# Kernel optimization log

Measured on AMD Instinct MI355X. Metric: run time of the kernel, lower is better.

## Reference

```python
import jax, jax.numpy as jnp
import numpy as np

B, S, E, D = 2, 1024, 1024, 2048
H, KV, HD = 8, 4, 256
SOFTCAP = 50.0
SCALE = 256.0 ** -0.5  # query_pre_attn_scalar ** -0.5
WINDOW = 512
EPS = 1e-6
THETA = 10000.0


def setup_inputs() -> dict:
    key = jax.random.key(0)
    ks = jax.random.split(key, 10)
    hidden_states = jax.random.normal(ks[0], (B, S, D), jnp.float32)
    encoder_hidden_states = jax.random.normal(ks[1], (B, E, D), jnp.float32)
    # two packed segments per sequence (position resets at S//2)
    position_ids = jnp.broadcast_to(
        jnp.concatenate([jnp.arange(S // 2), jnp.arange(S - S // 2)]), (B, S)
    ).astype(jnp.int32)
    decoder_attention_mask = jnp.ones((B, S), jnp.int32)
    encoder_attention_mask = jnp.broadcast_to(
        (jnp.arange(E) < (E - 64)).astype(jnp.int32), (B, E))
    # RoPE tables from position ids
    inv_freq = 1.0 / (THETA ** (jnp.arange(0, HD, 2, dtype=jnp.float32) / HD))
    freqs = position_ids.astype(jnp.float32)[..., None] * inv_freq  # [B,S,HD/2]
    emb = jnp.concatenate([freqs, freqs], axis=-1)  # [B,S,HD]
    cos, sin = jnp.cos(emb), jnp.sin(emb)
    wq = 0.02 * jax.random.normal(ks[2], (D, H * HD), jnp.float32)
    wk = 0.02 * jax.random.normal(ks[3], (D, KV * HD), jnp.float32)
    wv = 0.02 * jax.random.normal(ks[4], (D, KV * HD), jnp.float32)
    wo = 0.02 * jax.random.normal(ks[5], (H * HD, D), jnp.float32)
    q_norm_w = 0.1 * jax.random.normal(ks[6], (HD,), jnp.float32)
    k_norm_w = 0.1 * jax.random.normal(ks[7], (HD,), jnp.float32)
    return dict(hidden_states=hidden_states,
                encoder_hidden_states=encoder_hidden_states,
                cos=cos, sin=sin, wq=wq, wk=wk, wv=wv, wo=wo,
                q_norm_w=q_norm_w, k_norm_w=k_norm_w,
                decoder_attention_mask=decoder_attention_mask,
                encoder_attention_mask=encoder_attention_mask,
                position_ids=position_ids)


def _rms_norm(x, w):
    # GemmaRMSNorm: x * rsqrt(mean(x^2)+eps) * (1 + w)
    var = jnp.mean(x * x, axis=-1, keepdims=True)
    return x * jax.lax.rsqrt(var + EPS) * (1.0 + w)


def _rotate_half(x):
    h = x.shape[-1] // 2
    return jnp.concatenate([-x[..., h:], x[..., :h]], axis=-1)


def _build_merged_mask(dec_mask, enc_mask, position_ids):
    dm = dec_mask.astype(bool)
    em = enc_mask.astype(bool)
    Sq = dm.shape[1]
    causal = jnp.tril(jnp.ones((Sq, Sq), bool))
    # segment ids from non-increasing position resets (packing)
    reset = jnp.concatenate(
        [jnp.ones((dm.shape[0], 1), bool),
         position_ids[:, 1:] <= position_ids[:, :-1]], axis=1)
    seg = jnp.cumsum(reset.astype(jnp.int32), axis=1)
    block = seg[:, :, None] == seg[:, None, :]
    full_self = dm[:, None, :] & causal[None] & block  # [B,S,S]
    rows = jnp.arange(Sq)
    dist = rows[:, None] - rows[None, :]
    sliding = (dist >= 0) & (dist < WINDOW)
    self_mask = full_self & sliding[None]
    cross = jnp.broadcast_to(em[:, None, :], (dm.shape[0], Sq, em.shape[1]))
    return jnp.concatenate([self_mask, cross], axis=-1)[:, None]  # [B,1,S,S+E]


def reference(hidden_states, encoder_hidden_states, cos, sin, wq, wk, wv, wo,
              q_norm_w, k_norm_w, decoder_attention_mask,
              encoder_attention_mask, position_ids):
    Bq, Sq, _ = hidden_states.shape
    Ek = encoder_hidden_states.shape[1]
    q = (hidden_states @ wq).reshape(Bq, Sq, H, HD).transpose(0, 2, 1, 3)
    k_self = (hidden_states @ wk).reshape(Bq, Sq, KV, HD).transpose(0, 2, 1, 3)
    v_self = (hidden_states @ wv).reshape(Bq, Sq, KV, HD).transpose(0, 2, 1, 3)
    k_cross = (encoder_hidden_states @ wk).reshape(Bq, Ek, KV, HD).transpose(0, 2, 1, 3)
    v_cross = (encoder_hidden_states @ wv).reshape(Bq, Ek, KV, HD).transpose(0, 2, 1, 3)
    # QK RMSNorm (cross keys normalized but NOT rotated, matching source)
    q = _rms_norm(q, q_norm_w)
    k_self = _rms_norm(k_self, k_norm_w)
    k_cross = _rms_norm(k_cross, k_norm_w)
    c, s = cos[:, None, :, :], sin[:, None, :, :]
    q = q * c + _rotate_half(q) * s
    k_self = k_self * c + _rotate_half(k_self) * s
    k = jnp.concatenate([k_self, k_cross], axis=2)  # [B,KV,S+E,HD]
    v = jnp.concatenate([v_self, v_cross], axis=2)
    rep = H // KV
    k = jnp.repeat(k, rep, axis=1)
    v = jnp.repeat(v, rep, axis=1)
    mask = _build_merged_mask(decoder_attention_mask, encoder_attention_mask,
                              position_ids)
    scores = jnp.einsum('bhqd,bhkd->bhqk', q, k) * SCALE
    scores = SOFTCAP * jnp.tanh(scores / SOFTCAP)  # logit softcapping
    scores = jnp.where(mask, scores, jnp.float32(-1e30))
    attn = jax.nn.softmax(scores, axis=-1)
    out = jnp.einsum('bhqk,bhkd->bhqd', attn, v)
    out = out.transpose(0, 2, 1, 3).reshape(Bq, Sq, H * HD)
    return out @ wo
```

## Files before the change

kernel.cpp:

```cpp
#include <hip/hip_runtime.h>
#include <math.h>

#define B_ 2
#define S_ 1024
#define E_ 1024
#define D_ 2048
#define H_ 8
#define KV_ 4
#define HD_ 256
#define WINDOW_ 512u
#define SCALE_ 0.0625f
#define CAP_ 50.0f
#define EPS_ 1e-6f
#define CROSS_OK (-7)
#define KINV (-2147483647 - 1)

typedef __bf16 bf8_t __attribute__((ext_vector_type(8)));
typedef float fx4 __attribute__((ext_vector_type(4)));
#define MFMA16(a, b, c) __builtin_amdgcn_mfma_f32_16x16x32_bf16((a), (b), (c), 0, 0, 0)

typedef __attribute__((address_space(1))) unsigned int gas_u32;
typedef __attribute__((address_space(3))) unsigned int las_u32;
__device__ __forceinline__ void gl2lds16(const void* g, void* l) {
    __builtin_amdgcn_global_load_lds((const gas_u32*)g, (las_u32*)l, 16, 0, 0);
}

union U4 { __bf16 b[4]; unsigned long long u; };

__device__ __forceinline__ float pexp(float dot) {
    float e = __expf(dot * (2.0f * SCALE_ / CAP_));
    return __expf(-(2.0f * CAP_) / (e + 1.0f));
}

__global__ __launch_bounds__(256) void tobf16(const float* __restrict__ x,
                                              __bf16* __restrict__ y, int n4) {
    int i = blockIdx.x * 256 + threadIdx.x;
    if (i >= n4) return;
    float4 v = ((const float4*)x)[i];
    U4 p;
    p.b[0] = (__bf16)v.x; p.b[1] = (__bf16)v.y;
    p.b[2] = (__bf16)v.z; p.b[3] = (__bf16)v.w;
    *(unsigned long long*)&y[(size_t)i * 4] = p.u;
}

__global__ __launch_bounds__(256) void tsplit(const float* __restrict__ W,
                                              __bf16* __restrict__ Th,
                                              __bf16* __restrict__ Tl, int K, int N) {
    __shared__ float tile[32][33];
    const int t = threadIdx.x, tx = t & 31, ty = t >> 5;
    const int k0 = blockIdx.x * 32, n0 = blockIdx.y * 32;
#pragma unroll
    for (int r = 0; r < 4; ++r)
        tile[ty + r * 8][tx] = W[(size_t)(k0 + ty + r * 8) * N + n0 + tx];
    __syncthreads();
#pragma unroll
    for (int r = 0; r < 4; ++r) {
        float v = tile[tx][ty + r * 8];
        __bf16 h = (__bf16)v;
        size_t o = (size_t)(n0 + ty + r * 8) * K + k0 + tx;
        Th[o] = h;
        Tl[o] = (__bf16)(v - (float)h);
    }
}

template <int NPASS>
__device__ __forceinline__ void gemm_core2(
    const __bf16* __restrict__ Ah, const __bf16* __restrict__ Al,
    const __bf16* __restrict__ Bh, const __bf16* __restrict__ Bl,
    int row0, int col0, int K,
    __bf16* As0, __bf16* As1, __bf16* Bs0, __bf16* Bs1, fx4 (&acc)[4][4]) {
    const int tid = threadIdx.x, lane = tid & 63, wv = tid >> 6;
    const int l15 = lane & 15, lq = lane >> 4;
    const int wm = (wv >> 1) * 64, wn = (wv & 1) * 64;
    constexpr int WCNT = (NPASS == 1) ? 0x0F74 : (NPASS == 2) ? 0x0F76 : 0x0F78;

    auto stage = [&](int buf, int k0) {
#pragma unroll
        for (int s = 0; s < 2; ++s) {
            int ch = (wv * 2 + s) * 64 + lane;
            int r = ch >> 2, cp = ch & 3;
            int cl = (cp - ((r >> 1) & 3)) & 3;
            size_t ga = (size_t)(row0 + r) * K + k0 + cl * 8;
            size_t gb = (size_t)(col0 + r) * K + k0 + cl * 8;
            gl2lds16(Ah + ga, As0 + buf * 4096 + ch * 8);
            if (NPASS >= 3) gl2lds16(Al + ga, As1 + buf * 4096 + ch * 8);
            gl2lds16(Bh + gb, Bs0 + buf * 4096 + ch * 8);
            if (NPASS >= 2) gl2lds16(Bl + gb, Bs1 + buf * 4096 + ch * 8);
        }
    };

    stage(0, 0);
    for (int k0 = 0; k0 < K; k0 += 32) {
        const int buf = (k0 >> 5) & 1;
        const bool hasnext = (k0 + 32 < K);
        if (hasnext) stage(buf ^ 1, k0 + 32);
        if (hasnext) __builtin_amdgcn_s_waitcnt(WCNT);
        else         __builtin_amdgcn_s_waitcnt(0x0F70);
        __builtin_amdgcn_s_barrier();
        __builtin_amdgcn_sched_barrier(0);

        const __bf16* A0 = As0 + buf * 4096;
        const __bf16* A1 = As1 + buf * 4096;
        const __bf16* B0 = Bs0 + buf * 4096;
        const __bf16* B1 = Bs1 + buf * 4096;
        bf8_t ah[4], al[4], bh[4], bl[4];
#pragma unroll
        for (int i = 0; i < 4; ++i) {
            int row = wm + i * 16 + l15;
            int sl = row * 4 + ((lq + (row >> 1)) & 3);
            ah[i] = *(const bf8_t*)(A0 + sl * 8);
            if (NPASS >= 3) al[i] = *(const bf8_t*)(A1 + sl * 8);
        }
#pragma unroll
        for (int j = 0; j < 4; ++j) {
            int row = wn + j * 16 + l15;
            int sl = row * 4 + ((lq + (row >> 1)) & 3);
            bh[j] = *(const bf8_t*)(B0 + sl * 8);
            if (NPASS >= 2) bl[j] = *(const bf8_t*)(B1 + sl * 8);
        }
#pragma unroll
        for (int i = 0; i < 4; ++i)
#pragma unroll
            for (int j = 0; j < 4; ++j) {
                acc[i][j] = MFMA16(ah[i], bh[j], acc[i][j]);
                if (NPASS >= 2) acc[i][j] = MFMA16(ah[i], bl[j], acc[i][j]);
                if (NPASS >= 3) acc[i][j] = MFMA16(al[i], bh[j], acc[i][j]);
            }
        __builtin_amdgcn_sched_barrier(0);
        __builtin_amdgcn_s_barrier();
    }
}

__global__ __launch_bounds__(256) void gemm_proj(
    const __bf16* __restrict__ hsb, const __bf16* __restrict__ encb,
    const __bf16* __restrict__ BTh, const __bf16* __restrict__ BTl,
    float* __restrict__ qf32, float* __restrict__ ksf, float* __restrict__ kcf,
    __bf16* __restrict__ vtS, __bf16* __restrict__ vtC) {
    __shared__ __bf16 As0[8192], Bs0[8192], Bs1[8192];
    const int bx = blockIdx.x, row0 = blockIdx.y * 128;
    const __bf16* A;
    float* Ck; __bf16* Cv; int col0;
    if (bx < 32) { A = hsb;  col0 = bx * 128;               Ck = ksf; Cv = vtS; }
    else         { A = encb; col0 = (bx - 32) * 128 + 2048; Ck = kcf; Cv = vtC; }
    fx4 acc[4][4];
#pragma unroll
    for (int i = 0; i < 4; ++i)
#pragma unroll
        for (int j = 0; j < 4; ++j) acc[i][j] = (fx4){0.f, 0.f, 0.f, 0.f};
    if (col0 >= 3072)
        gemm_core2<2>(A, nullptr, BTh, BTl, row0, col0, D_, As0, nullptr, Bs0, Bs1, acc);
    else
        gemm_core2<1>(A, nullptr, BTh, BTl, row0, col0, D_, As0, nullptr, Bs0, Bs1, acc);

    const int tid = threadIdx.x, lane = tid & 63, wv = tid >> 6;
    const int l15 = lane & 15, lq = lane >> 4;
    const int wm = (wv >> 1) * 64, wn = (wv & 1) * 64;
    const int mode = (col0 < 2048) ? 0 : (col0 < 3072 ? 1 : 2);
#pragma unroll
    for (int i = 0; i < 4; ++i)
#pragma unroll
        for (int j = 0; j < 4; ++j) {
            int mb = row0 + wm + i * 16 + lq * 4;
            int n = col0 + wn + j * 16 + l15;
            if (mode == 0) {
#pragma unroll
                for (int r = 0; r < 4; ++r)
                    qf32[(size_t)(mb + r) * 2048 + n] = acc[i][j][r];
            } else if (mode == 1) {
                int nk = n - 2048;
#pragma unroll
                for (int r = 0; r < 4; ++r)
                    Ck[(size_t)(mb + r) * 1024 + nk] = acc[i][j][r];
            } else {
                int nv = n - 3072;
                int b = mb >> 10, s = mb & 1023;
                int kv = nv >> 8, d = nv & 255;
                U4 pk;
#pragma unroll
                for (int r = 0; r < 4; ++r) pk.b[r] = (__bf16)acc[i][j][r];
                *(unsigned long long*)&Cv[((size_t)(b * KV_ + kv) * HD_ + d) * 1024 + s] = pk.u;
            }
        }
}

__global__ __launch_bounds__(256) void gemm_out(
    const __bf16* __restrict__ Ah, const __bf16* __restrict__ Al,
    const __bf16* __restrict__ Bh, const __bf16* __restrict__ Bl,
    float* __restrict__ C) {
    __shared__ __bf16 As0[8192], As1[8192], Bs0[8192], Bs1[8192];
    const int row0 = blockIdx.y * 128, col0 = blockIdx.x * 128;
    fx4 acc[4][4];
#pragma unroll
    for (int i = 0; i < 4; ++i)
#pragma unroll
        for (int j = 0; j < 4; ++j) acc[i][j] = (fx4){0.f, 0.f, 0.f, 0.f};
    gemm_core2<3>(Ah, Al, Bh, Bl, row0, col0, 2048, As0, As1, Bs0, Bs1, acc);
    const int tid = threadIdx.x, lane = tid & 63, wv = tid >> 6;
    const int l15 = lane & 15, lq = lane >> 4;
    const int wm = (wv >> 1) * 64, wn = (wv & 1) * 64;
#pragma unroll
    for (int i = 0; i < 4; ++i)
#pragma unroll
        for (int j = 0; j < 4; ++j) {
            int mb = row0 + wm + i * 16 + lq * 4;
            int n = col0 + wn + j * 16 + l15;
#pragma unroll
            for (int r = 0; r < 4; ++r)
                C[(size_t)(mb + r) * 2048 + n] = acc[i][j][r];
        }
}

__global__ __launch_bounds__(256) void rmsnorm_rope(const float* __restrict__ x,
                                                    __bf16* __restrict__ out,
                                                    const float* __restrict__ w,
                                                    const float* __restrict__ cs,
                                                    const float* __restrict__ sn,
                                                    int nheads, int do_rope, int trans) {
    const int tid = threadIdx.x;
    const size_t base = (size_t)blockIdx.x * HD_;
    float v = x[base + tid];
    float ss = v * v;
#pragma unroll
    for (int off = 32; off; off >>= 1) ss += __shfl_down(ss, off);
    __shared__ float red[4];
    __shared__ float ybuf[HD_];
    const int lane = tid & 63, wvi = tid >> 6;
    if (lane == 0) red[wvi] = ss;
    __syncthreads();
    float tot = red[0] + red[1] + red[2] + red[3];
    float scale = rsqrtf(tot * (1.0f / HD_) + EPS_);
    float y = v * scale * (1.0f + w[tid]);
    const int m = blockIdx.x / nheads;
    if (do_rope) {
        ybuf[tid] = y;
        __syncthreads();
        float rot = (tid < HD_ / 2) ? -ybuf[tid + HD_ / 2] : ybuf[tid - HD_ / 2];
        size_t coff = (size_t)m * HD_;
        y = y * cs[coff + tid] + rot * sn[coff + tid];
    }
    size_t oidx;
    if (trans) {
        int hh = blockIdx.x % nheads;
        int b = m >> 10, s = m & 1023;
        oidx = ((size_t)(b * nheads + hh) * 1024 + s) * HD_ + tid;
    } else {
        oidx = base + tid;
    }
    out[oidx] = (__bf16)y;
}

__global__ void segscan(const int* __restrict__ pos, const int* __restrict__ dm,
                        const int* __restrict__ em, int* __restrict__ seg,
                        int* __restrict__ ki) {
    const int b = blockIdx.x, s = threadIdx.x;
    __shared__ int sh[1024];
    int p = pos[b * S_ + s];
    int r = (s == 0) ? 1 : (p <= pos[b * S_ + s - 1] ? 1 : 0);
    sh[s] = r;
    __syncthreads();
    for (int off = 1; off < 1024; off <<= 1) {
        int v = sh[s];
        int u = (s >= off) ? sh[s - off] : 0;
        __syncthreads();
        sh[s] = v + u;
        __syncthreads();
    }
    int sv = sh[s];
    seg[b * S_ + s] = sv;
    ki[b * 2048 + s] = dm[b * S_ + s] ? sv : KINV;
    ki[b * 2048 + 1024 + s] = em[b * E_ + s] ? CROSS_OK : KINV;
}

__global__ __launch_bounds__(128, 1) void attn_fused(
    const __bf16* __restrict__ qb,
    const __bf16* __restrict__ kb,
    const __bf16* __restrict__ kcb,
    const __bf16* __restrict__ vtS,
    const __bf16* __restrict__ vtC,
    const int* __restrict__ seg, const int* __restrict__ ki,
    __bf16* __restrict__ aH, __bf16* __restrict__ aL) {
    __shared__ __bf16 Ks[2][8192];
    __shared__ __bf16 Vs[2][8192];
    __shared__ __bf16 Ps[2][640];
    __shared__ int kinfoS[1600];
    const int tid = threadIdx.x, lane = tid & 63, wv = tid >> 6;
    const int l15 = lane & 15, lq = lane >> 4;
    const int g = blockIdx.x & 7;
    const int b = g >> 2, kv = g & 3;
    const int rest = blockIdx.x >> 3;
    const int qt = rest >> 1, h = kv * 2 + (rest & 1);
    const int s0 = qt * 32;
    const int lo = (s0 >= 512) ? ((s0 - 511) & ~31) : 0;
    const int nself = (s0 + 32 - lo) >> 5;
    const int nselfK = nself * 32;
    const int nt = nself + 32;

    for (int i = tid; i < nselfK + 1024; i += 128)
        kinfoS[i] = (i < nselfK) ? ki[b * 2048 + lo + i]
                                 : ki[b * 2048 + 1024 + (i - nselfK)];
    __syncthreads();

    const int qpos = s0 + wv * 16 + l15;
    bf8_t qf[8];
    const __bf16* qrow = qb + ((size_t)(b * S_ + qpos) * H_ + h) * HD_;
#pragma unroll
    for (int f = 0; f < 8; ++f) qf[f] = *(const bf8_t*)(qrow + f * 32 + lq * 8);
    const int segq = seg[b * S_ + qpos];

    const __bf16* KbS = kb  + (size_t)(b * KV_ + kv) * (1024 * 256);
    const __bf16* VbS = vtS + (size_t)(b * KV_ + kv) * (256 * 1024);
    const __bf16* KbC = kcb + (size_t)(b * KV_ + kv) * (1024 * 256);
    const __bf16* VbC = vtC + (size_t)(b * KV_ + kv) * (256 * 1024);

    const __bf16 *Kt, *Vt; int kio, kt0, sf;
    auto tinfo = [&](int i) {
        if (i < nself) { sf = 1; kt0 = lo + i * 32;
                         Kt = KbS + (size_t)kt0 * 256; Vt = VbS + kt0; kio = i * 32; }
        else { sf = 0; int j = i - nself; kt0 = j * 32;
               Kt = KbC + (size_t)kt0 * 256; Vt = VbC + kt0; kio = nselfK + j * 32; }
    };
    auto stage = [&](int buf) {
#pragma unroll
        for (int r = 0; r < 8; ++r) {
            int cid = r * 128 + tid;
            int key = cid >> 5, c = cid & 31;
            gl2lds16(Kt + key * 256 + (((c ^ (key & 7))) << 3), &Ks[buf][cid * 8]);
        }
#pragma unroll
        for (int r = 0; r < 8; ++r) {
            int cid = r * 128 + tid;
            int d = cid >> 2, kc = cid & 3;
            gl2lds16(Vt + (size_t)d * 1024 + ((kc ^ ((d >> 1) & 3)) << 3), &Vs[buf][cid * 8]);
        }
    };

    fx4 accO[16];
#pragma unroll
    for (int j = 0; j < 16; ++j) accO[j] = (fx4){0.f, 0.f, 0.f, 0.f};
    float lsum = 0.f;
    const int swzk = l15 & 7;
    const int swzv = lq ^ ((l15 >> 1) & 3);

    tinfo(0);
    stage(0);
    for (int i = 0; i < nt; ++i) {
        const int kio_c = kio, kt0_c = kt0, sf_c = sf;
        const int hasnext = (i + 1 < nt);
        if (hasnext) { tinfo(i + 1); stage((i + 1) & 1); }
        if (hasnext) __builtin_amdgcn_s_waitcnt(0x4F70);
        else         __builtin_amdgcn_s_waitcnt(0x0F70);
        __builtin_amdgcn_s_barrier();
        __builtin_amdgcn_sched_barrier(0);

        const __bf16* Ksb = Ks[i & 1];
        const __bf16* Vsb = Vs[i & 1];
        fx4 sc0 = (fx4){0.f, 0.f, 0.f, 0.f}, sc1 = (fx4){0.f, 0.f, 0.f, 0.f};
#pragma unroll
        for (int f = 0; f < 8; ++f) {
            bf8_t k0 = *(const bf8_t*)&Ksb[(l15 * 32 + ((f * 4 + lq) ^ swzk)) * 8];
            bf8_t k1 = *(const bf8_t*)&Ksb[((16 + l15) * 32 + ((f * 4 + lq) ^ swzk)) * 8];
            sc0 = MFMA16(k0, qf[f], sc0);
            sc1 = MFMA16(k1, qf[f], sc1);
        }
        int4 ki0 = *(const int4*)&kinfoS[kio_c + lq * 4];
        int4 ki1 = *(const int4*)&kinfoS[kio_c + 16 + lq * 4];
        int ka0[4] = {ki0.x, ki0.y, ki0.z, ki0.w};
        int ka1[4] = {ki1.x, ki1.y, ki1.z, ki1.w};
        const int tgt = sf_c ? segq : CROSS_OK;
        U4 p0, p1;
#pragma unroll
        for (int r = 0; r < 4; ++r) {
            int key0 = kt0_c + lq * 4 + r;
            float e0 = pexp(sc0[r]);
            float e1 = pexp(sc1[r]);
            bool ok0 = (ka0[r] == tgt) && (!sf_c || (unsigned)(qpos - key0) < WINDOW_);
            bool ok1 = (ka1[r] == tgt) && (!sf_c || (unsigned)(qpos - key0 - 16) < WINDOW_);
            float v0 = ok0 ? e0 : 0.f;
            float v1 = ok1 ? e1 : 0.f;
            lsum += v0 + v1;
            p0.b[r] = (__bf16)v0;
            p1.b[r] = (__bf16)v1;
        }
        *(unsigned long long*)&Ps[wv][l15 * 40 + lq * 4] = p0.u;
        *(unsigned long long*)&Ps[wv][l15 * 40 + 16 + lq * 4] = p1.u;
        bf8_t pf = *(const bf8_t*)&Ps[wv][l15 * 40 + lq * 8];
#pragma unroll
        for (int j = 0; j < 16; ++j) {
            bf8_t vb = *(const bf8_t*)&Vsb[((j * 16 + l15) * 4 + swzv) * 8];
            accO[j] = MFMA16(pf, vb, accO[j]);
        }
        __builtin_amdgcn_sched_barrier(0);
        __builtin_amdgcn_s_barrier();
    }

    lsum += __shfl_xor(lsum, 16, 64);
    lsum += __shfl_xor(lsum, 32, 64);
    float inv[4];
#pragma unroll
    for (int r = 0; r < 4; ++r) inv[r] = 1.0f / __shfl(lsum, lq * 4 + r, 64);
#pragma unroll
    for (int j = 0; j < 16; ++j)
#pragma unroll
        for (int r = 0; r < 4; ++r) {
            float o = accO[j][r] * inv[r];
            size_t idx = (size_t)(b * S_ + s0 + wv * 16 + lq * 4 + r) * 2048 +
                         h * 256 + j * 16 + l15;
            __bf16 hi = (__bf16)o;
            aH[idx] = hi;
            aL[idx] = (__bf16)(o - (float)hi);
        }
}

extern "C" void kernel_launch(void* const* d_in, const int* in_sizes, int n_in,
                              void* d_out, int out_size, void* d_ws, size_t ws_size,
                              hipStream_t stream) {
    (void)in_sizes; (void)n_in; (void)out_size; (void)ws_size;
    const float* hs  = (const float*)d_in[0];
    const float* enc = (const float*)d_in[1];
    const float* cs  = (const float*)d_in[2];
    const float* sn  = (const float*)d_in[3];
    const float* wq  = (const float*)d_in[4];
    const float* wk  = (const float*)d_in[5];
    const float* wv  = (const float*)d_in[6];
    const float* wo  = (const float*)d_in[7];
    const float* qnw = (const float*)d_in[8];
    const float* knw = (const float*)d_in[9];
    const int* dm    = (const int*)d_in[10];
    const int* em    = (const int*)d_in[11];
    const int* pos   = (const int*)d_in[12];
    float* out = (float*)d_out;

    char* ws = (char*)d_ws;
    const size_t MB = 1ull << 20;
    __bf16* hs_bf   = (__bf16*)(ws + 0 * MB);
    __bf16* enc_bf  = (__bf16*)(ws + 8 * MB);
    __bf16* wqkvTH  = (__bf16*)(ws + 16 * MB);
    __bf16* wqkvTL  = (__bf16*)(ws + 32 * MB);
    __bf16* woTH    = (__bf16*)(ws + 48 * MB);
    __bf16* woTL    = (__bf16*)(ws + 56 * MB);
    float*  qf32    = (float*)(ws + 64 * MB);
    float*  ksf     = (float*)(ws + 80 * MB);
    float*  kcf     = (float*)(ws + 88 * MB);
    __bf16* k_bf    = (__bf16*)(ws + 104 * MB);
    __bf16* kc_bf   = (__bf16*)(ws + 108 * MB);
    __bf16* vtS     = (__bf16*)(ws + 112 * MB);
    __bf16* vtC     = (__bf16*)(ws + 116 * MB);
    int*    seg     = (int*)(ws + 120 * MB);
    int*    kinfo   = (int*)(ws + 121 * MB);
    __bf16* q_bf    = (__bf16*)(ws + 124 * MB);
    __bf16* aoutH   = (__bf16*)(ws + 0 * MB);
    __bf16* aoutL   = (__bf16*)(ws + 9 * MB);

    const int M = B_ * S_;

    tobf16<<<4096, 256, 0, stream>>>(hs, hs_bf, M * D_ / 4);
    tobf16<<<4096, 256, 0, stream>>>(enc, enc_bf, M * D_ / 4);
    tsplit<<<dim3(64, 64), 256, 0, stream>>>(wq, wqkvTH, wqkvTL, D_, 2048);
    tsplit<<<dim3(64, 32), 256, 0, stream>>>(wk, wqkvTH + (size_t)2048 * 2048,
                                             wqkvTL + (size_t)2048 * 2048, D_, 1024);
    tsplit<<<dim3(64, 32), 256, 0, stream>>>(wv, wqkvTH + (size_t)3072 * 2048,
                                             wqkvTL + (size_t)3072 * 2048, D_, 1024);
    tsplit<<<dim3(64, 64), 256, 0, stream>>>(wo, woTH, woTL, 2048, D_);

    gemm_proj<<<dim3(48, 16), 256, 0, stream>>>(hs_bf, enc_bf, wqkvTH, wqkvTL,
                                                qf32, ksf, kcf, vtS, vtC);

    rmsnorm_rope<<<16384, 256, 0, stream>>>(qf32, q_bf, qnw, cs, sn, H_, 1, 0);
    rmsnorm_rope<<<8192, 256, 0, stream>>>(ksf, k_bf, knw, cs, sn, KV_, 1, 1);
    rmsnorm_rope<<<8192, 256, 0, stream>>>(kcf, kc_bf, knw, cs, sn, KV_, 0, 1);
    segscan<<<B_, 1024, 0, stream>>>(pos, dm, em, seg, kinfo);

    attn_fused<<<512, 128, 0, stream>>>(q_bf, k_bf, kc_bf, vtS, vtC, seg, kinfo,
                                        aoutH, aoutL);

    gemm_out<<<dim3(16, 16), 256, 0, stream>>>(aoutH, aoutL, woTH, woTL, out);
}
```

Measured before the change: 449.1 us.

## Split attention into separate self and cross key passes with combine kernel

Result: faster. 428.6 us (-4.6%).

```diff
diff --git a/kernel.cpp b/kernel.cpp
--- a/kernel.cpp
+++ b/kernel.cpp
@@ -271,33 +271,43 @@
     ki[b * 2048 + 1024 + s] = em[b * E_ + s] ? CROSS_OK : KINV;
 }
 
-__global__ __launch_bounds__(128, 1) void attn_fused(
+__global__ __launch_bounds__(256, 1) void attn_part(
     const __bf16* __restrict__ qb,
     const __bf16* __restrict__ kb,
     const __bf16* __restrict__ kcb,
     const __bf16* __restrict__ vtS,
     const __bf16* __restrict__ vtC,
     const int* __restrict__ seg, const int* __restrict__ ki,
-    __bf16* __restrict__ aH, __bf16* __restrict__ aL) {
+    float* __restrict__ accS, float* __restrict__ accC,
+    float* __restrict__ lsS, float* __restrict__ lsC) {
     __shared__ __bf16 Ks[2][8192];
     __shared__ __bf16 Vs[2][8192];
-    __shared__ __bf16 Ps[2][640];
-    __shared__ int kinfoS[1600];
+    __shared__ __bf16 Ps[4][640];
+    __shared__ int kinfoS[1024];
     const int tid = threadIdx.x, lane = tid & 63, wv = tid >> 6;
     const int l15 = lane & 15, lq = lane >> 4;
-    const int g = blockIdx.x & 7;
+    const int bid = blockIdx.x;
+    const int role = bid >> 8;
+    const int g = bid & 7;
     const int b = g >> 2, kv = g & 3;
-    const int rest = blockIdx.x >> 3;
+    const int rest = (bid >> 3) & 31;
     const int qt = rest >> 1, h = kv * 2 + (rest & 1);
-    const int s0 = qt * 32;
-    const int lo = (s0 >= 512) ? ((s0 - 511) & ~31) : 0;
-    const int nself = (s0 + 32 - lo) >> 5;
-    const int nselfK = nself * 32;
-    const int nt = nself + 32;
-
-    for (int i = tid; i < nselfK + 1024; i += 128)
-        kinfoS[i] = (i < nselfK) ? ki[b * 2048 + lo + i]
-                                 : ki[b * 2048 + 1024 + (i - nselfK)];
+    const int s0 = qt * 64;
+
+    int lo = 0, nt = 32;
+    const __bf16 *Kbase, *Vbase;
+    if (role == 0) {
+        lo = (s0 >= 512) ? ((s0 - 511) & ~31) : 0;
+        nt = (s0 + 64 - lo) >> 5;
+        Kbase = kb + (size_t)(b * KV_ + kv) * (1024 * 256);
+        Vbase = vtS + (size_t)(b * KV_ + kv) * (256 * 1024);
+    } else {
+        Kbase = kcb + (size_t)(b * KV_ + kv) * (1024 * 256);
+        Vbase = vtC + (size_t)(b * KV_ + kv) * (256 * 1024);
+    }
+    const int nk = nt * 32;
+    const int kiofs = b * 2048 + (role ? 1024 : lo);
+    for (int i = tid; i < nk; i += 256) kinfoS[i] = ki[kiofs + i];
     __syncthreads();
 
     const int qpos = s0 + wv * 16 + l15;
@@ -305,32 +315,23 @@
     const __bf16* qrow = qb + ((size_t)(b * S_ + qpos) * H_ + h) * HD_;
 #pragma unroll
     for (int f = 0; f < 8; ++f) qf[f] = *(const bf8_t*)(qrow + f * 32 + lq * 8);
-    const int segq = seg[b * S_ + qpos];
-
-    const __bf16* KbS = kb  + (size_t)(b * KV_ + kv) * (1024 * 256);
-    const __bf16* VbS = vtS + (size_t)(b * KV_ + kv) * (256 * 1024);
-    const __bf16* KbC = kcb + (size_t)(b * KV_ + kv) * (1024 * 256);
-    const __bf16* VbC = vtC + (size_t)(b * KV_ + kv) * (256 * 1024);
-
-    const __bf16 *Kt, *Vt; int kio, kt0, sf;
-    auto tinfo = [&](int i) {
-        if (i < nself) { sf = 1; kt0 = lo + i * 32;
-                         Kt = KbS + (size_t)kt0 * 256; Vt = VbS + kt0; kio = i * 32; }
-        else { sf = 0; int j = i - nself; kt0 = j * 32;
-               Kt = KbC + (size_t)kt0 * 256; Vt = VbC + kt0; kio = nselfK + j * 32; }
-    };
-    auto stage = [&](int buf) {
-#pragma unroll
-        for (int r = 0; r < 8; ++r) {
-            int cid = r * 128 + tid;
+    const int tgt = role ? CROSS_OK : seg[b * S_ + qpos];
+
+    auto stage = [&](int buf, int t) {
+        const __bf16* Kt = Kbase + (size_t)(lo + t * 32) * 256;
+        const __bf16* Vt = Vbase + (lo + t * 32);
+#pragma unroll
+        for (int r = 0; r < 4; ++r) {
+            int cid = r * 256 + tid;
             int key = cid >> 5, c = cid & 31;
             gl2lds16(Kt + key * 256 + (((c ^ (key & 7))) << 3), &Ks[buf][cid * 8]);
         }
 #pragma unroll
-        for (int r = 0; r < 8; ++r) {
-            int cid = r * 128 + tid;
+        for (int r = 0; r < 4; ++r) {
+            int cid = r * 256 + tid;
             int d = cid >> 2, kc = cid & 3;
-            gl2lds16(Vt + (size_t)d * 1024 + ((kc ^ ((d >> 1) & 3)) << 3), &Vs[buf][cid * 8]);
+            gl2lds16(Vt + (size_t)d * 1024 + ((kc ^ ((d >> 1) & 3)) << 3),
+                     &Vs[buf][cid * 8]);
         }
     };
 
@@ -341,13 +342,13 @@
     const int swzk = l15 & 7;
     const int swzv = lq ^ ((l15 >> 1) & 3);
 
-    tinfo(0);
-    stage(0);
+    stage(0, 0);
     for (int i = 0; i < nt; ++i) {
-        const int kio_c = kio, kt0_c = kt0, sf_c = sf;
-        const int hasnext = (i + 1 < nt);
-        if (hasnext) { tinfo(i + 1); stage((i + 1) & 1); }
-        if (hasnext) __builtin_amdgcn_s_waitcnt(0x4F70);
+        const int kt0_c = lo + i * 32;
+        const int kio_c = i * 32;
+        const bool hasnext = (i + 1 < nt);
+        if (hasnext) stage((i + 1) & 1, i + 1);
+        if (hasnext) __builtin_amdgcn_s_waitcnt(0x0F78);
         else         __builtin_amdgcn_s_waitcnt(0x0F70);
         __builtin_amdgcn_s_barrier();
         __builtin_amdgcn_sched_barrier(0);
@@ -366,15 +367,14 @@
         int4 ki1 = *(const int4*)&kinfoS[kio_c + 16 + lq * 4];
         int ka0[4] = {ki0.x, ki0.y, ki0.z, ki0.w};
         int ka1[4] = {ki1.x, ki1.y, ki1.z, ki1.w};
-        const int tgt = sf_c ? segq : CROSS_OK;
         U4 p0, p1;
 #pragma unroll
         for (int r = 0; r < 4; ++r) {
             int key0 = kt0_c + lq * 4 + r;
             float e0 = pexp(sc0[r]);
             float e1 = pexp(sc1[r]);
-            bool ok0 = (ka0[r] == tgt) && (!sf_c || (unsigned)(qpos - key0) < WINDOW_);
-            bool ok1 = (ka1[r] == tgt) && (!sf_c || (unsigned)(qpos - key0 - 16) < WINDOW_);
+            bool ok0 = (ka0[r] == tgt) && (role || (unsigned)(qpos - key0) < WINDOW_);
+            bool ok1 = (ka1[r] == tgt) && (role || (unsigned)(qpos - key0 - 16) < WINDOW_);
             float v0 = ok0 ? e0 : 0.f;
             float v1 = ok1 ? e1 : 0.f;
             lsum += v0 + v1;
@@ -395,20 +395,41 @@
 
     lsum += __shfl_xor(lsum, 16, 64);
     lsum += __shfl_xor(lsum, 32, 64);
-    float inv[4];
-#pragma unroll
-    for (int r = 0; r < 4; ++r) inv[r] = 1.0f / __shfl(lsum, lq * 4 + r, 64);
+    float* accT = role ? accC : accS;
+    float* lsT  = role ? lsC  : lsS;
+    if (lq == 0) lsT[(size_t)(b * S_ + qpos) * 8 + h] = lsum;
 #pragma unroll
     for (int j = 0; j < 16; ++j)
 #pragma unroll
         for (int r = 0; r < 4; ++r) {
-            float o = accO[j][r] * inv[r];
             size_t idx = (size_t)(b * S_ + s0 + wv * 16 + lq * 4 + r) * 2048 +
                          h * 256 + j * 16 + l15;
-            __bf16 hi = (__bf16)o;
-            aH[idx] = hi;
-            aL[idx] = (__bf16)(o - (float)hi);
-        }
+            accT[idx] = accO[j][r];
+        }
+}
+
+__global__ __launch_bounds__(256) void combine(
+    const float* __restrict__ aS, const float* __restrict__ aC,
+    const float* __restrict__ lS, const float* __restrict__ lC,
+    __bf16* __restrict__ aH, __bf16* __restrict__ aL) {
+    int i = blockIdx.x * 256 + threadIdx.x;
+    size_t base = (size_t)i * 4;
+    int row = (int)(base >> 11);
+    int h = (int)((base >> 8) & 7);
+    float inv = 1.0f / (lS[row * 8 + h] + lC[row * 8 + h]);
+    float4 a = ((const float4*)aS)[i];
+    float4 c = ((const float4*)aC)[i];
+    float o[4] = {(a.x + c.x) * inv, (a.y + c.y) * inv,
+                  (a.z + c.z) * inv, (a.w + c.w) * inv};
+    U4 ph, pl;
+#pragma unroll
+    for (int r = 0; r < 4; ++r) {
+        __bf16 hi = (__bf16)o[r];
+        ph.b[r] = hi;
+        pl.b[r] = (__bf16)(o[r] - (float)hi);
+    }
+    *(unsigned long long*)&aH[base] = ph.u;
+    *(unsigned long long*)&aL[base] = pl.u;
 }
 
 extern "C" void kernel_launch(void* const* d_in, const int* in_sizes, int n_in,
@@ -450,6 +471,10 @@
     __bf16* q_bf    = (__bf16*)(ws + 124 * MB);
     __bf16* aoutH   = (__bf16*)(ws + 0 * MB);
     __bf16* aoutL   = (__bf16*)(ws + 9 * MB);
+    float*  accS    = (float*)(ws + 64 * MB);
+    float*  accC    = (float*)(ws + 81 * MB);
+    float*  lsS     = (float*)(ws + 98 * MB);
+    float*  lsC     = (float*)(ws + 99 * MB);
 
     const int M = B_ * S_;
 
@@ -470,8 +495,9 @@
     rmsnorm_rope<<<8192, 256, 0, stream>>>(kcf, kc_bf, knw, cs, sn, KV_, 0, 1);
     segscan<<<B_, 1024, 0, stream>>>(pos, dm, em, seg, kinfo);
 
-    attn_fused<<<512, 128, 0, stream>>>(q_bf, k_bf, kc_bf, vtS, vtC, seg, kinfo,
-                                        aoutH, aoutL);
+    attn_part<<<512, 256, 0, stream>>>(q_bf, k_bf, kc_bf, vtS, vtC, seg, kinfo,
+                                       accS, accC, lsS, lsC);
+    combine<<<4096, 256, 0, stream>>>(accS, accC, lsS, lsC, aoutH, aoutL);
 
     gemm_out<<<dim3(16, 16), 256, 0, stream>>>(aoutH, aoutL, woTH, woTL, out);
 }
```
